# Optimization experiments

Hardware: AMD Instinct MI355X
Metric: run time of the kernel (lower is better)

Reference implementation:

```python
import jax, jax.numpy as jnp
import numpy as np

B, S, D, H = 2, 2048, 1024, 16
DK = D // H  # 64
SCALE = DK ** (-0.5)  # NOTE: module divides by this, i.e. multiplies scores by sqrt(DK)


def setup_inputs() -> dict:
    key = jax.random.key(0)
    ks = jax.random.split(key, 9)
    std = D ** (-0.5)
    return {
        "x": jax.random.normal(ks[0], (B, S, D), dtype=jnp.float32),
        "attention_mask": jnp.ones((B, S), dtype=jnp.int32),
        "Wq": jax.random.normal(ks[1], (D, D), dtype=jnp.float32) * std,
        "bq": jnp.zeros((D,), dtype=jnp.float32),
        "Wk": jax.random.normal(ks[2], (D, D), dtype=jnp.float32) * std,
        "bk": jnp.zeros((D,), dtype=jnp.float32),
        "Wv": jax.random.normal(ks[3], (D, D), dtype=jnp.float32) * std,
        "bv": jnp.zeros((D,), dtype=jnp.float32),
        "Wo": jax.random.normal(ks[4], (D, D), dtype=jnp.float32) * std,
        "bo": jnp.zeros((D,), dtype=jnp.float32),
    }


def _split_heads(t):
    # [B, S, D] -> [B, H, S, DK]
    return t.reshape(B, S, H, DK).transpose(0, 2, 1, 3)


def reference(x, attention_mask, Wq, bq, Wk, bk, Wv, bv, Wo, bo):
    q = _split_heads(x @ Wq.T + bq)
    k = _split_heads(x @ Wk.T + bk)
    v = _split_heads(x @ Wv.T + bv)

    # faithful to source: sim = (q @ k^T) / scale with scale = dk**-0.5
    sim = jnp.einsum("bhqd,bhkd->bhqk", q, k) / SCALE

    # key-padding mask: positions where attention_mask == 0 are masked out
    neg = jnp.finfo(sim.dtype).min
    keep = attention_mask.astype(bool)[:, None, None, :]  # [B,1,1,S]
    sim = jnp.where(keep, sim, neg)

    attn = jax.nn.softmax(sim, axis=-1)  # dropout is identity at inference
    out = jnp.einsum("bhqk,bhkd->bhqd", attn, v)
    out = out.transpose(0, 2, 1, 3).reshape(B, S, D)  # merge heads
    return out @ Wo.T + bo
```

## Files before the change

### kernel.cpp

```cpp
#include <hip/hip_runtime.h>
#include <hip/hip_bf16.h>
#include <math.h>

#define BB 2
#define SS 2048
#define DD 1024
#define HH 16
#define DKK 64
#define BH (BB * HH)

typedef __bf16 bf16_t;
typedef _Float16 f16_t;
typedef __attribute__((ext_vector_type(8))) _Float16 f16x8;
typedef __attribute__((ext_vector_type(4))) _Float16 f16x4;
typedef __attribute__((ext_vector_type(4))) float f32x4;
typedef __attribute__((ext_vector_type(4))) int i32x4;
typedef __attribute__((ext_vector_type(2))) int i32x2;

#define GLD_LDS(gp, lp) __builtin_amdgcn_global_load_lds( \
    (const __attribute__((address_space(1))) void*)(gp),  \
    (__attribute__((address_space(3))) void*)(lp), 16, 0, 0)

static __device__ __forceinline__ int pkrtz(float a, float b) {
    auto h = __builtin_amdgcn_cvt_pkrtz(a, b);
    return __builtin_bit_cast(int, h);
}

__global__ void cast_x_flags(const float* __restrict__ in, f16_t* __restrict__ out,
                             const int* __restrict__ mask, int* __restrict__ flags, int n) {
    int i = blockIdx.x * blockDim.x + threadIdx.x;
    int stride = gridDim.x * blockDim.x;
    for (; i < n; i += stride) out[i] = (f16_t)in[i];
    if (blockIdx.x == 0 && threadIdx.x < BB * (SS / 128)) {
        int f = threadIdx.x;
        int b = f / (SS / 128), t = f % (SS / 128);
        const int* p = mask + b * SS + t * 128;
        int all = 1;
        for (int j = 0; j < 128; ++j) all &= (p[j] != 0);
        flags[f] = all;
    }
}

__global__ void cast_wqk(const float* __restrict__ Wq, const float* __restrict__ Wk,
                         f16_t* __restrict__ hi, f16_t* __restrict__ lo, int nw) {
    int i = blockIdx.x * blockDim.x + threadIdx.x;
    int stride = gridDim.x * blockDim.x;
    for (; i < 2 * nw; i += stride) {
        float v = (i < nw) ? Wq[i] : Wk[i - nw];
        f16_t h = (f16_t)v;
        hi[i] = h;
        lo[i] = (f16_t)(v - (float)h);
    }
}

__global__ void cast_wvo(const float* __restrict__ Wv, const float* __restrict__ Wo,
                         f16_t* __restrict__ wv, f16_t* __restrict__ wo, int nw) {
    int i = blockIdx.x * blockDim.x + threadIdx.x;
    int stride = gridDim.x * blockDim.x;
    for (; i < 2 * nw; i += stride) {
        if (i < nw) wv[i] = (f16_t)Wv[i];
        else        wo[i - nw] = (f16_t)Wo[i - nw];
    }
}

__global__ __launch_bounds__(256) void gemm_qkv(const f16_t* __restrict__ Af,
                                                const f16_t* __restrict__ Wqkh,
                                                const f16_t* __restrict__ Wqkl,
                                                const f16_t* __restrict__ Wvf,
                                                const float* __restrict__ bq,
                                                const float* __restrict__ bk,
                                                const float* __restrict__ bv,
                                                f16_t* __restrict__ q_o,
                                                f16_t* __restrict__ k_o,
                                                f16_t* __restrict__ vt_o,
                                                int K) {
    __shared__ __align__(16) f16_t sA[4096];
    __shared__ __align__(16) f16_t sB0[4096];
    __shared__ __align__(16) f16_t sB1[4096];

    const int tid  = threadIdx.x;
    const int wv   = tid >> 6;
    const int lane = tid & 63;
    const int quad = lane >> 4;
    const int l15  = lane & 15;
    const int wr   = wv >> 1;
    const int wc   = wv & 1;
    const int row0 = blockIdx.y * 128;
    const int col0 = blockIdx.x * 128;
    const bool isV = (col0 >= 2048);

    const f16_t* B0 = isV ? (Wvf + (long)(col0 - 2048) * K) : (Wqkh + (long)col0 * K);
    const f16_t* B1 = isV ? nullptr : (Wqkl + (long)col0 * K);

    f32x4 acc[4][4] = {};

    const int srow = tid >> 2;
    const int scol = (tid & 3) * 8;
    const long aoff = (long)(row0 + srow) * K + scol;
    const long boff = (long)srow * K + scol;

    if (isV) {
#pragma unroll 1
        for (int kb = 0; kb < K; kb += 32) {
#pragma unroll
            for (int p = 0; p < 2; ++p) {
                const long go = (long)p * 64 * K + kb;
                const int lo = p * 2048 + wv * 512;
                GLD_LDS(Af + aoff + go, sA + lo);
                GLD_LDS(B0 + boff + go, sB0 + lo);
            }
            __syncthreads();
            f16x8 af[4];
#pragma unroll
            for (int mt = 0; mt < 4; ++mt)
                af[mt] = *(const f16x8*)&sA[(wr * 64 + mt * 16 + l15) * 32 + quad * 8];
#pragma unroll
            for (int nt = 0; nt < 4; ++nt) {
                f16x8 b0 = *(const f16x8*)&sB0[(wc * 64 + nt * 16 + l15) * 32 + quad * 8];
#pragma unroll
                for (int mt = 0; mt < 4; ++mt)
                    acc[mt][nt] = __builtin_amdgcn_mfma_f32_16x16x32_f16(af[mt], b0, acc[mt][nt], 0, 0, 0);
            }
            __syncthreads();
        }
    } else {
#pragma unroll 1
        for (int kb = 0; kb < K; kb += 32) {
#pragma unroll
            for (int p = 0; p < 2; ++p) {
                const long go = (long)p * 64 * K + kb;
                const int lo = p * 2048 + wv * 512;
                GLD_LDS(Af + aoff + go, sA + lo);
                GLD_LDS(B0 + boff + go, sB0 + lo);
                GLD_LDS(B1 + boff + go, sB1 + lo);
            }
            __syncthreads();
            f16x8 af[4];
#pragma unroll
            for (int mt = 0; mt < 4; ++mt)
                af[mt] = *(const f16x8*)&sA[(wr * 64 + mt * 16 + l15) * 32 + quad * 8];
#pragma unroll
            for (int nt = 0; nt < 4; ++nt) {
                f16x8 b0 = *(const f16x8*)&sB0[(wc * 64 + nt * 16 + l15) * 32 + quad * 8];
                f16x8 b1 = *(const f16x8*)&sB1[(wc * 64 + nt * 16 + l15) * 32 + quad * 8];
#pragma unroll
                for (int mt = 0; mt < 4; ++mt) {
                    acc[mt][nt] = __builtin_amdgcn_mfma_f32_16x16x32_f16(af[mt], b0, acc[mt][nt], 0, 0, 0);
                    acc[mt][nt] = __builtin_amdgcn_mfma_f32_16x16x32_f16(af[mt], b1, acc[mt][nt], 0, 0, 0);
                }
            }
            __syncthreads();
        }
    }

    if (isV) {
#pragma unroll
        for (int nt = 0; nt < 4; ++nt) {
            const int colv = (col0 - 2048) + wc * 64 + nt * 16 + l15;
            const float bvv = bv[colv];
            const int hq = colv >> 6, dk = colv & 63;
#pragma unroll
            for (int mt = 0; mt < 4; ++mt) {
                const int grow0 = row0 + wr * 64 + mt * 16 + quad * 4;
                const int bq2 = grow0 >> 11;
                const int s0  = grow0 & (SS - 1);
                f16x4 pk;
#pragma unroll
                for (int r = 0; r < 4; ++r) pk[r] = (f16_t)(acc[mt][nt][r] + bvv);
                *(f16x4*)(vt_o + ((long)(bq2 * HH + hq) * DKK + dk) * SS + s0) = pk;
            }
        }
    } else {
        const bool isK = (col0 >= 1024);
        const float* bias = isK ? bk : bq;
        f16_t* op = isK ? k_o : q_o;
#pragma unroll
        for (int nt = 0; nt < 4; ++nt) {
            const int gcol = (col0 & 1023) + wc * 64 + nt * 16 + l15;
            const float bvv = bias[gcol];
            const int hq = gcol >> 6, dk = gcol & 63;
#pragma unroll
            for (int mt = 0; mt < 4; ++mt) {
                const int grow0 = row0 + wr * 64 + mt * 16 + quad * 4;
#pragma unroll
                for (int r = 0; r < 4; ++r) {
                    int grow = grow0 + r;
                    float vvv = acc[mt][nt][r] + bvv;
                    long off = (((long)(grow >> 11) * HH + hq) * SS + (grow & (SS - 1))) * DKK + dk;
                    op[off] = (f16_t)vvv;
                }
            }
        }
    }
}

__global__ __launch_bounds__(256) void gemm_o(const f16_t* __restrict__ Ah,
                                              const f16_t* __restrict__ Bhp,
                                              const float* __restrict__ bias,
                                              float* __restrict__ outf,
                                              int N, int K) {
    __shared__ __align__(16) f16_t lds[2048 + 4096];
    f16_t* Ash = lds;
    f16_t* Bsh = lds + 2048;

    const int tid  = threadIdx.x;
    const int wv   = tid >> 6;
    const int lane = tid & 63;
    const int quad = lane >> 4;
    const int l15  = lane & 15;
    const int wr   = wv >> 1;
    const int wc   = wv & 1;
    const int row0 = blockIdx.y * 64;
    const int col0 = blockIdx.x * 128;

    f32x4 acc[2][4] = {};

    const int srow = lane >> 2;
    const int scol = (lane & 3) * 8;
    const f16_t* gA  = Ah  + (long)(row0 + wv * 16 + srow) * K + scol;
    const f16_t* gB0 = Bhp + (long)(col0 + wv * 16 + srow) * K + scol;
    const f16_t* gB1 = Bhp + (long)(col0 + (wv + 4) * 16 + srow) * K + scol;
    f16_t* lA  = Ash + wv * 512;
    f16_t* lB0 = Bsh + wv * 512;
    f16_t* lB1 = Bsh + (wv + 4) * 512;

#pragma unroll 1
    for (int kb = 0; kb < K; kb += 32) {
        GLD_LDS(gA + kb, lA);
        GLD_LDS(gB0 + kb, lB0);
        GLD_LDS(gB1 + kb, lB1);
        __syncthreads();

        f16x8 af[2];
#pragma unroll
        for (int mt = 0; mt < 2; ++mt)
            af[mt] = *(const f16x8*)&Ash[(wr * 32 + mt * 16 + l15) * 32 + quad * 8];
#pragma unroll
        for (int nt = 0; nt < 4; ++nt) {
            f16x8 bh = *(const f16x8*)&Bsh[(wc * 64 + nt * 16 + l15) * 32 + quad * 8];
#pragma unroll
            for (int mt = 0; mt < 2; ++mt)
                acc[mt][nt] = __builtin_amdgcn_mfma_f32_16x16x32_f16(af[mt], bh, acc[mt][nt], 0, 0, 0);
        }
        __syncthreads();
    }

#pragma unroll
    for (int mt = 0; mt < 2; ++mt) {
#pragma unroll
        for (int nt = 0; nt < 4; ++nt) {
            const int gcol  = col0 + wc * 64 + nt * 16 + l15;
            const float bvv = bias[gcol];
            const int grow0 = row0 + wr * 32 + mt * 16 + quad * 4;
#pragma unroll
            for (int r = 0; r < 4; ++r)
                outf[(long)(grow0 + r) * N + gcol] = acc[mt][nt][r] + bvv;
        }
    }
}

__global__ __launch_bounds__(256) void attn_mfma7(const f16_t* __restrict__ Qp,
                                                  const f16_t* __restrict__ Kp,
                                                  const f16_t* __restrict__ Vtp,
                                                  const int* __restrict__ mask,
                                                  const int* __restrict__ flags,
                                                  f16_t* __restrict__ ctx,
                                                  int seq_len) {
    __shared__ __align__(16) f16_t Ksh[2][4096];
    __shared__ __align__(16) f16_t Vsh[2][4096];

    const int tid  = threadIdx.x;
    const int wv   = tid >> 6;
    const int lane = tid & 63;
    const int quad = lane >> 4;
    const int l15  = lane & 15;
    const int bh   = blockIdx.y;
    const int b    = bh >> 4;
    const int h    = bh & 15;
    const int q0   = blockIdx.x * 64 + wv * 16;

    const long kb = (long)bh * SS * DKK;

    f16x8 qf[2];
    {
        const f16_t* pq = Qp + kb + (long)(q0 + l15) * DKK + quad * 8;
        qf[0] = *(const f16x8*)pq;
        qf[1] = *(const f16x8*)(pq + 32);
        const f16_t qs = (f16_t)(8.0f * 1.44269504088896f);
#pragma unroll
        for (int j = 0; j < 8; ++j) { qf[0][j] *= qs; qf[1][j] *= qs; }
    }

    f32x4 o[4];
#pragma unroll
    for (int r = 0; r < 4; ++r) o[r] = (f32x4){0.f, 0.f, 0.f, 0.f};
    float lsum = 0.f;
    float m = -1e30f;

    const int* mrow = mask + b * SS;
    const int* frow = flags + b * (SS / 128);

    const int srow8 = lane >> 3;
    const int gcolB = ((lane & 7) ^ srow8) * 8;

#pragma unroll 1
    for (int kt = 0; kt < seq_len; kt += 128) {
#pragma unroll
        for (int c = 0; c < 2; ++c) {
            const int kc = kt + c * 64;
#pragma unroll
            for (int p = 0; p < 2; ++p) {
                const int i = wv * 2 + p;
                const int row = i * 8 + srow8;
                GLD_LDS(Kp + kb + (long)(kc + row) * DKK + gcolB, &Ksh[c][i * 512]);
                GLD_LDS(Vtp + kb + (long)row * SS + kc + gcolB, &Vsh[c][i * 512]);
            }
        }
        __syncthreads();

        f32x4 s[8];
#pragma unroll
        for (int nt = 0; nt < 8; ++nt) s[nt] = (f32x4){0.f, 0.f, 0.f, 0.f};
#pragma unroll
        for (int nt = 0; nt < 8; ++nt) {
            const int c = nt >> 2;
            const int kr = (nt & 3) * 16 + l15;
#pragma unroll
            for (int dt = 0; dt < 2; ++dt) {
                f16x8 kf = *(const f16x8*)&Ksh[c][kr * 64 + (((dt * 4 + quad) ^ (l15 & 7)) << 3)];
                s[nt] = __builtin_amdgcn_mfma_f32_16x16x32_f16(kf, qf[dt], s[nt], 0, 0, 0);
            }
        }

        if (!frow[kt >> 7]) {
#pragma unroll
            for (int nt = 0; nt < 8; ++nt) {
                i32x4 kp = *(const i32x4*)&mrow[kt + nt * 16 + quad * 4];
#pragma unroll
                for (int r = 0; r < 4; ++r)
                    s[nt][r] = kp[r] ? s[nt][r] : -1e30f;
            }
        }

        f32x4 mx;
#pragma unroll
        for (int r = 0; r < 4; ++r)
            mx[r] = fmaxf(fmaxf(fmaxf(s[0][r], s[1][r]), fmaxf(s[2][r], s[3][r])),
                          fmaxf(fmaxf(s[4][r], s[5][r]), fmaxf(s[6][r], s[7][r])));
        float tm = fmaxf(fmaxf(mx[0], mx[1]), fmaxf(mx[2], mx[3]));
        tm = fmaxf(tm, __shfl_xor(tm, 16));
        tm = fmaxf(tm, __shfl_xor(tm, 32));

        const float mn = fmaxf(m, tm);
        if (__any(tm > m)) {
            const float alpha = exp2f(m - mn);
            lsum *= alpha;
            float a4[4];
#pragma unroll
            for (int r = 0; r < 4; ++r)
                a4[r] = __shfl(alpha, quad * 4 + r);
#pragma unroll
            for (int t = 0; t < 4; ++t)
#pragma unroll
                for (int r = 0; r < 4; ++r) o[t][r] *= a4[r];
        }
        m = mn;

#pragma unroll
        for (int nt = 0; nt < 8; ++nt) {
            const int c = nt >> 2;
            float p0 = exp2f(s[nt][0] - mn);
            float p1 = exp2f(s[nt][1] - mn);
            float p2 = exp2f(s[nt][2] - mn);
            float p3 = exp2f(s[nt][3] - mn);
            lsum += (p0 + p1) + (p2 + p3);
            i32x2 pp;
            pp[0] = pkrtz(p0, p1);
            pp[1] = pkrtz(p2, p3);
            f16x4 paf = __builtin_bit_cast(f16x4, pp);
            const int vcol = ((((nt & 3) * 2 + (quad >> 1)) ^ (l15 & 7)) << 3) + ((quad & 1) << 2);
#pragma unroll
            for (int t = 0; t < 4; ++t) {
                f16x4 vB = *(const f16x4*)&Vsh[c][(t * 16 + l15) * 64 + vcol];
                o[t] = __builtin_amdgcn_mfma_f32_16x16x16f16(paf, vB, o[t], 0, 0, 0);
            }
        }
        __syncthreads();
    }

    lsum += __shfl_xor(lsum, 16);
    lsum += __shfl_xor(lsum, 32);
    float inv[4];
#pragma unroll
    for (int r = 0; r < 4; ++r)
        inv[r] = 1.0f / __shfl(lsum, quad * 4 + r);
#pragma unroll
    for (int t = 0; t < 4; ++t) {
        int d = t * 16 + l15;
#pragma unroll
        for (int r = 0; r < 4; ++r) {
            int tok = b * SS + q0 + quad * 4 + r;
            ctx[(long)tok * DD + h * DKK + d] = (f16_t)(o[t][r] * inv[r]);
        }
    }
}

extern "C" void kernel_launch(void* const* d_in, const int* in_sizes, int n_in,
                              void* d_out, int out_size, void* d_ws, size_t ws_size,
                              hipStream_t stream) {
    const float* x  = (const float*)d_in[0];
    const int* mask = (const int*)d_in[1];
    const float* Wq = (const float*)d_in[2];
    const float* bq = (const float*)d_in[3];
    const float* Wk = (const float*)d_in[4];
    const float* bk = (const float*)d_in[5];
    const float* Wv = (const float*)d_in[6];
    const float* bv = (const float*)d_in[7];
    const float* Wo = (const float*)d_in[8];
    const float* bo = (const float*)d_in[9];
    float* out = (float*)d_out;

    const long NX = (long)BB * SS * DD;
    const long NW = (long)DD * DD;

    char* ws = (char*)d_ws;
    f16_t* xf   = (f16_t*)ws; ws += NX * 2;
    f16_t* wqkh = (f16_t*)ws; ws += 2 * NW * 2;
    f16_t* wqkl = (f16_t*)ws; ws += 2 * NW * 2;
    f16_t* wvf  = (f16_t*)ws; ws += NW * 2;
    f16_t* wof  = (f16_t*)ws; ws += NW * 2;
    f16_t* qf   = (f16_t*)ws; ws += NX * 2;
    f16_t* kf   = (f16_t*)ws; ws += NX * 2;
    f16_t* vt   = (f16_t*)ws; ws += NX * 2;
    f16_t* ctx  = (f16_t*)ws; ws += NX * 2;
    int*   flg  = (int*)ws;   ws += 64 * 4;

    cast_x_flags<<<2048, 256, 0, stream>>>(x, xf, mask, flg, (int)NX);
    cast_wqk<<<2048, 256, 0, stream>>>(Wq, Wk, wqkh, wqkl, (int)NW);
    cast_wvo<<<2048, 256, 0, stream>>>(Wv, Wo, wvf, wof, (int)NW);

    dim3 gqkv(3 * DD / 128, (BB * SS) / 128);
    gemm_qkv<<<gqkv, 256, 0, stream>>>(xf, wqkh, wqkl, wvf, bq, bk, bv, qf, kf, vt, DD);

    dim3 agrid(SS / 64, BH);
    attn_mfma7<<<agrid, 256, 0, stream>>>(qf, kf, vt, mask, flg, ctx, SS);

    dim3 go(DD / 128, (BB * SS) / 64);
    gemm_o<<<go, 256, 0, stream>>>(ctx, wof, bo, out, DD, DD);
}
```

Baseline: 284.7 us.

## Double-buffer K/V tiles in attention and compute row sums with MFMA

The attention kernel now keeps two LDS buffers for K and V. It prefetches the next 128-key tile with global_load_lds while computing on the current one, and drops the trailing barrier in each iteration. The softmax denominator is accumulated with an extra MFMA against a vector of ones, which replaces the per-lane scalar adds and the final cross-lane shuffle reduction. LDS use per block doubles to 64KB, which can lower the number of resident blocks per CU.

```diff
diff --git a/kernel.cpp b/kernel.cpp
--- a/kernel.cpp
+++ b/kernel.cpp
@@ -259,15 +259,15 @@
     }
 }
 
-__global__ __launch_bounds__(256) void attn_mfma7(const f16_t* __restrict__ Qp,
+__global__ __launch_bounds__(256) void attn_mfma8(const f16_t* __restrict__ Qp,
                                                   const f16_t* __restrict__ Kp,
                                                   const f16_t* __restrict__ Vtp,
                                                   const int* __restrict__ mask,
                                                   const int* __restrict__ flags,
                                                   f16_t* __restrict__ ctx,
                                                   int seq_len) {
-    __shared__ __align__(16) f16_t Ksh[2][4096];
-    __shared__ __align__(16) f16_t Vsh[2][4096];
+    __shared__ __align__(16) f16_t Ksh[2][2][4096];
+    __shared__ __align__(16) f16_t Vsh[2][2][4096];
 
     const int tid  = threadIdx.x;
     const int wv   = tid >> 6;
@@ -291,10 +291,14 @@
         for (int j = 0; j < 8; ++j) { qf[0][j] *= qs; qf[1][j] *= qs; }
     }
 
-    f32x4 o[4];
+    f16x4 ones4;
+#pragma unroll
+    for (int j = 0; j < 4; ++j) ones4[j] = (f16_t)1.0f;
+
+    f32x4 o[4], lacc;
 #pragma unroll
     for (int r = 0; r < 4; ++r) o[r] = (f32x4){0.f, 0.f, 0.f, 0.f};
-    float lsum = 0.f;
+    lacc = (f32x4){0.f, 0.f, 0.f, 0.f};
     float m = -1e30f;
 
     const int* mrow = mask + b * SS;
@@ -302,21 +306,38 @@
 
     const int srow8 = lane >> 3;
     const int gcolB = ((lane & 7) ^ srow8) * 8;
+    const int NT = seq_len >> 7;
+
+#pragma unroll
+    for (int c = 0; c < 2; ++c) {
+#pragma unroll
+        for (int p = 0; p < 2; ++p) {
+            const int i = wv * 2 + p;
+            const int row = i * 8 + srow8;
+            GLD_LDS(Kp + kb + (long)(c * 64 + row) * DKK + gcolB, &Ksh[0][c][i * 512]);
+            GLD_LDS(Vtp + kb + (long)row * SS + c * 64 + gcolB, &Vsh[0][c][i * 512]);
+        }
+    }
 
 #pragma unroll 1
-    for (int kt = 0; kt < seq_len; kt += 128) {
-#pragma unroll
-        for (int c = 0; c < 2; ++c) {
-            const int kc = kt + c * 64;
-#pragma unroll
-            for (int p = 0; p < 2; ++p) {
-                const int i = wv * 2 + p;
-                const int row = i * 8 + srow8;
-                GLD_LDS(Kp + kb + (long)(kc + row) * DKK + gcolB, &Ksh[c][i * 512]);
-                GLD_LDS(Vtp + kb + (long)row * SS + kc + gcolB, &Vsh[c][i * 512]);
-            }
-        }
+    for (int tt = 0; tt < NT; ++tt) {
+        const int cur = tt & 1;
+        const int kt = tt << 7;
         __syncthreads();
+
+        if (tt + 1 < NT) {
+            const int kn = (tt + 1) << 7;
+#pragma unroll
+            for (int c = 0; c < 2; ++c) {
+#pragma unroll
+                for (int p = 0; p < 2; ++p) {
+                    const int i = wv * 2 + p;
+                    const int row = i * 8 + srow8;
+                    GLD_LDS(Kp + kb + (long)(kn + c * 64 + row) * DKK + gcolB, &Ksh[cur ^ 1][c][i * 512]);
+                    GLD_LDS(Vtp + kb + (long)row * SS + kn + c * 64 + gcolB, &Vsh[cur ^ 1][c][i * 512]);
+                }
+            }
+        }
 
         f32x4 s[8];
 #pragma unroll
@@ -327,7 +348,7 @@
             const int kr = (nt & 3) * 16 + l15;
 #pragma unroll
             for (int dt = 0; dt < 2; ++dt) {
-                f16x8 kf = *(const f16x8*)&Ksh[c][kr * 64 + (((dt * 4 + quad) ^ (l15 & 7)) << 3)];
+                f16x8 kf = *(const f16x8*)&Ksh[cur][c][kr * 64 + (((dt * 4 + quad) ^ (l15 & 7)) << 3)];
                 s[nt] = __builtin_amdgcn_mfma_f32_16x16x32_f16(kf, qf[dt], s[nt], 0, 0, 0);
             }
         }
@@ -354,7 +375,6 @@
         const float mn = fmaxf(m, tm);
         if (__any(tm > m)) {
             const float alpha = exp2f(m - mn);
-            lsum *= alpha;
             float a4[4];
 #pragma unroll
             for (int r = 0; r < 4; ++r)
@@ -363,6 +383,8 @@
             for (int t = 0; t < 4; ++t)
 #pragma unroll
                 for (int r = 0; r < 4; ++r) o[t][r] *= a4[r];
+#pragma unroll
+            for (int r = 0; r < 4; ++r) lacc[r] *= a4[r];
         }
         m = mn;
 
@@ -373,27 +395,23 @@
             float p1 = exp2f(s[nt][1] - mn);
             float p2 = exp2f(s[nt][2] - mn);
             float p3 = exp2f(s[nt][3] - mn);
-            lsum += (p0 + p1) + (p2 + p3);
             i32x2 pp;
             pp[0] = pkrtz(p0, p1);
             pp[1] = pkrtz(p2, p3);
             f16x4 paf = __builtin_bit_cast(f16x4, pp);
+            lacc = __builtin_amdgcn_mfma_f32_16x16x16f16(paf, ones4, lacc, 0, 0, 0);
             const int vcol = ((((nt & 3) * 2 + (quad >> 1)) ^ (l15 & 7)) << 3) + ((quad & 1) << 2);
 #pragma unroll
             for (int t = 0; t < 4; ++t) {
-                f16x4 vB = *(const f16x4*)&Vsh[c][(t * 16 + l15) * 64 + vcol];
+                f16x4 vB = *(const f16x4*)&Vsh[cur][c][(t * 16 + l15) * 64 + vcol];
                 o[t] = __builtin_amdgcn_mfma_f32_16x16x16f16(paf, vB, o[t], 0, 0, 0);
             }
         }
-        __syncthreads();
-    }
-
-    lsum += __shfl_xor(lsum, 16);
-    lsum += __shfl_xor(lsum, 32);
+    }
+
     float inv[4];
 #pragma unroll
-    for (int r = 0; r < 4; ++r)
-        inv[r] = 1.0f / __shfl(lsum, quad * 4 + r);
+    for (int r = 0; r < 4; ++r) inv[r] = 1.0f / lacc[r];
 #pragma unroll
     for (int t = 0; t < 4; ++t) {
         int d = t * 16 + l15;
@@ -443,7 +461,7 @@
     gemm_qkv<<<gqkv, 256, 0, stream>>>(xf, wqkh, wqkl, wvf, bq, bk, bv, qf, kf, vt, DD);
 
     dim3 agrid(SS / 64, BH);
-    attn_mfma7<<<agrid, 256, 0, stream>>>(qf, kf, vt, mask, flg, ctx, SS);
+    attn_mfma8<<<agrid, 256, 0, stream>>>(qf, kf, vt, mask, flg, ctx, SS);
 
     dim3 go(DD / 128, (BB * SS) / 64);
     gemm_o<<<go, 256, 0, stream>>>(ctx, wof, bo, out, DD, DD);
```

Measured after the change: 288.1 us. No clear change (+1.2%).
